# Kernel optimization log

Hardware: AMD Instinct MI355X
Metric: run time of the kernel (lower is better)

The kernel has to match this reference:

```python
import jax, jax.numpy as jnp
import numpy as np

B, S, D, H = 2, 2048, 1024, 16
HD = D // H  # head dim = 64


def setup_inputs() -> dict:
    key = jax.random.key(0)
    ks = jax.random.split(key, 11)
    s = 0.02
    return {
        "query": jax.random.normal(ks[0], (B, S, D), jnp.float32),
        "key": jax.random.normal(ks[1], (B, S, D), jnp.float32),
        "value": jax.random.normal(ks[2], (B, S, D), jnp.float32),
        "Wq": jax.random.normal(ks[3], (D, D), jnp.float32) * s,
        "bq": jnp.zeros((D,), jnp.float32),
        "Wk": jax.random.normal(ks[4], (D, D), jnp.float32) * s,
        "bk": jnp.zeros((D,), jnp.float32),
        "Wv": jax.random.normal(ks[5], (D, D), jnp.float32) * s,
        "bv": jnp.zeros((D,), jnp.float32),
        "Wo": jax.random.normal(ks[6], (D, D), jnp.float32) * s,
        "bo": jnp.zeros((D,), jnp.float32),
    }


def reference(query, key, value, Wq, bq, Wk, bk, Wv, bv, Wo, bo):
    # Linear projections (torch Linear: x @ W^T + b; here W stored as [in, out])
    q = query @ Wq + bq  # [B,S,D]
    k = key @ Wk + bk
    v = value @ Wv + bv
    # split heads -> [B,H,S,HD]
    q = q.reshape(B, S, H, HD).transpose(0, 2, 1, 3)
    k = k.reshape(B, S, H, HD).transpose(0, 2, 1, 3)
    v = v.reshape(B, S, H, HD).transpose(0, 2, 1, 3)
    scores = jnp.einsum("bhqd,bhkd->bhqk", q, k) / jnp.sqrt(jnp.float32(HD))
    probs = jax.nn.softmax(scores, axis=-1)
    # dropout is identity at inference
    ctx = jnp.einsum("bhqk,bhkd->bhqd", probs, v)
    ctx = ctx.transpose(0, 2, 1, 3).reshape(B, S, D)
    return ctx @ Wo + bo
```

## Files before the change

kernel.cpp:

```cpp
#include <hip/hip_runtime.h>
#include <hip/hip_bf16.h>

#define BB 2
#define SS 2048
#define DD 1024
#define HH 16
#define HD 64
#define MM (BB*SS)

typedef __attribute__((ext_vector_type(8))) short bf16x8;
typedef __attribute__((ext_vector_type(4))) float f32x4;

static __device__ inline unsigned short f2bf(float x) {
    unsigned int u = __float_as_uint(x);
    unsigned int r = (u + 0x7fffu + ((u >> 16) & 1u)) >> 16;
    return (unsigned short)r;
}

static __device__ inline unsigned pack2bf(float lo, float hi) {
    union { __hip_bfloat162 h; unsigned u; } c;
    c.h = __float22bfloat162_rn(make_float2(lo, hi));
    return c.u;
}

static __device__ inline f32x4 mfma16(bf16x8 a, bf16x8 b, f32x4 c) {
    return __builtin_amdgcn_mfma_f32_16x16x32_bf16(a, b, c, 0, 0, 0);
}

static __device__ inline float fast_exp2(float x) {
    return __builtin_amdgcn_exp2f(x);
}

typedef __attribute__((address_space(3))) unsigned int lds_u32;
typedef const __attribute__((address_space(1))) unsigned int glb_u32;
static __device__ inline void async_ld16(const void* g, void* l) {
    __builtin_amdgcn_global_load_lds((glb_u32*)g, (lds_u32*)l, 16, 0, 0);
}

struct PrepArgs {
    const float* csrc[3];
    unsigned short* cdst[3];
    const float* wsrc[4];
    unsigned short* wdst[4];
};
__global__ __launch_bounds__(256) void prep_inputs(PrepArgs args) {
    const int z = blockIdx.z;
    const int t = threadIdx.x;
    if (z < 3) {
        const float* in = args.csrc[z];
        unsigned short* out = args.cdst[z];
        int chunk = (blockIdx.y * 32 + blockIdx.x) * 4096;
#pragma unroll
        for (int r = 0; r < 4; r++) {
            int i = chunk + r * 1024 + t * 4;
            float4 v = *(const float4*)(in + i);
            uint2 o;
            o.x = pack2bf(v.x, v.y);
            o.y = pack2bf(v.z, v.w);
            *(uint2*)(out + i) = o;
        }
    } else {
        __shared__ float tile[32][33];
        const float* in = args.wsrc[z - 3];
        unsigned short* out = args.wdst[z - 3];
        int c0 = blockIdx.x * 32, r0 = blockIdx.y * 32;
        int x = t & 31, y0 = t >> 5;
        for (int yy = y0; yy < 32; yy += 8)
            tile[yy][x] = in[(size_t)(r0 + yy) * DD + c0 + x];
        __syncthreads();
        for (int yy = y0; yy < 32; yy += 8)
            out[(size_t)(c0 + yy) * DD + r0 + x] = f2bf(tile[x][yy]);
    }
}

struct QKVArgs {
    const unsigned short* A[3];
    const unsigned short* Bt[3];
    const float* bias[3];
    unsigned short* C[3];
};

#define QSCALE 0.1803368801111204f

#define NBUF 4
#define NT (DD / 32)

__global__ __launch_bounds__(512, 2) void gemm_qkv(QKVArgs args) {
    __shared__ alignas(16) unsigned short AS[NBUF][256 * 32];
    __shared__ alignas(16) unsigned short BS[NBUF][256 * 32];
    const int z = blockIdx.z;
    const float scale = (z == 0) ? QSCALE : 1.0f;
    const unsigned short* __restrict__ A = args.A[z];
    const unsigned short* __restrict__ Bt = args.Bt[z];
    const float* __restrict__ bias = args.bias[z];
    unsigned short* __restrict__ C = args.C[z];
    const int K = DD, N = DD;
    const int t = threadIdx.x;
    const int lane = t & 63, wave = t >> 6;
    const int quad = lane >> 4, l15 = lane & 15;
    const int wm = wave & 1, wn = wave >> 1;
    const int m0 = blockIdx.y * 256, n0 = blockIdx.x * 256;

    const int srow = wave * 16 + (lane >> 2);
    const int sslot = (lane & 3) ^ ((lane >> 3) & 3);
    const unsigned short* gA0 = A + (size_t)(m0 + srow) * K + sslot * 8;
    const unsigned short* gA1 = gA0 + (size_t)128 * K;
    const unsigned short* gB0 = Bt + (size_t)(n0 + srow) * K + sslot * 8;
    const unsigned short* gB1 = gB0 + (size_t)128 * K;
    const int rlo = wave * 512;
    const int rhi = wave * 512 + 4096;

    const int swzq = quad ^ ((l15 >> 1) & 3);

    auto stage = [&](int kt) {
        const int b = kt & (NBUF - 1);
        const size_t ko = (size_t)kt * 32;
        async_ld16(gA0 + ko, &AS[b][rlo]);
        async_ld16(gA1 + ko, &AS[b][rhi]);
        async_ld16(gB0 + ko, &BS[b][rlo]);
        async_ld16(gB1 + ko, &BS[b][rhi]);
    };

    stage(0); stage(1); stage(2);

    f32x4 acc[8][4];
#pragma unroll
    for (int i = 0; i < 8; i++)
#pragma unroll
        for (int j = 0; j < 4; j++) acc[i][j] = (f32x4){0.f, 0.f, 0.f, 0.f};

#pragma unroll 4
    for (int kt = 0; kt < NT; ++kt) {
        if (kt < NT - 2)       asm volatile("s_waitcnt vmcnt(8)" ::: "memory");
        else if (kt == NT - 2) asm volatile("s_waitcnt vmcnt(4)" ::: "memory");
        else                   asm volatile("s_waitcnt vmcnt(0)" ::: "memory");
        __builtin_amdgcn_s_barrier();
        if (kt + 3 < NT) stage(kt + 3);

        const unsigned short* Ab = AS[kt & (NBUF - 1)];
        const unsigned short* Bb = BS[kt & (NBUF - 1)];
        bf16x8 af[8], bfr[4];
#pragma unroll
        for (int i = 0; i < 8; i++)
            af[i] = *(const bf16x8*)&Ab[(wm * 128 + i * 16 + l15) * 32 + swzq * 8];
#pragma unroll
        for (int j = 0; j < 4; j++)
            bfr[j] = *(const bf16x8*)&Bb[(wn * 64 + j * 16 + l15) * 32 + swzq * 8];

        __builtin_amdgcn_s_setprio(1);
#pragma unroll
        for (int i = 0; i < 8; i++)
#pragma unroll
            for (int j = 0; j < 4; j++)
                acc[i][j] = mfma16(af[i], bfr[j], acc[i][j]);
        __builtin_amdgcn_s_setprio(0);
    }

    if (z == 2) {
#pragma unroll
        for (int j = 0; j < 4; j++) {
            int col = n0 + wn * 64 + j * 16 + l15;
            float bv = bias[col];
#pragma unroll
            for (int i = 0; i < 8; i++) {
                int rowb = m0 + wm * 128 + i * 16 + quad * 4;
                int b = rowb >> 11, s = rowb & (SS - 1);
                uint2 w;
                w.x = pack2bf(acc[i][j][0] + bv, acc[i][j][1] + bv);
                w.y = pack2bf(acc[i][j][2] + bv, acc[i][j][3] + bv);
                *(uint2*)(C + (size_t)b * DD * SS + (size_t)col * SS + s) = w;
            }
        }
    } else {
#pragma unroll
        for (int j = 0; j < 4; j++) {
            int col = n0 + wn * 64 + j * 16 + l15;
            float bv = bias[col];
#pragma unroll
            for (int i = 0; i < 8; i++) {
                int rowb = m0 + wm * 128 + i * 16 + quad * 4;
#pragma unroll
                for (int rr = 0; rr < 4; rr++) {
                    float v = (acc[i][j][rr] + bv) * scale;
                    C[(size_t)(rowb + rr) * N + col] = f2bf(v);
                }
            }
        }
    }
}

__global__ __launch_bounds__(256) void gemm_out(const unsigned short* __restrict__ A,
                                                const unsigned short* __restrict__ Bt,
                                                const float* __restrict__ bias,
                                                float* __restrict__ C) {
    __shared__ alignas(16) unsigned short As[128 * 32];
    __shared__ alignas(16) unsigned short Bs[64 * 32];
    const int t = threadIdx.x;
    const int lane = t & 63, wave = t >> 6;
    const int quad = lane >> 4, l15 = lane & 15;
    const int m0 = blockIdx.y * 128, n0 = blockIdx.x * 64;
    const int K = DD, N = DD;

    const unsigned short* gA = A + (size_t)(m0 + wave * 16 + (lane >> 2)) * K + (lane & 3) * 8;
    const unsigned short* gB = Bt + (size_t)(n0 + wave * 16 + (lane >> 2)) * K + (lane & 3) * 8;
    unsigned short* lA0 = &As[(wave * 16) * 32];
    unsigned short* lA1 = &As[(wave * 16 + 64) * 32];
    unsigned short* lB0 = &Bs[(wave * 16) * 32];

    f32x4 acc[2][4];
#pragma unroll
    for (int i = 0; i < 2; i++)
#pragma unroll
        for (int j = 0; j < 4; j++) acc[i][j] = (f32x4){0.f, 0.f, 0.f, 0.f};

    for (int k0 = 0; k0 < K; k0 += 32) {
        __syncthreads();
        async_ld16(gA + k0, lA0);
        async_ld16(gA + (size_t)64 * K + k0, lA1);
        async_ld16(gB + k0, lB0);
        __syncthreads();

        bf16x8 af[2], bfr[4];
#pragma unroll
        for (int i = 0; i < 2; i++)
            af[i] = *(const bf16x8*)&As[(wave * 32 + i * 16 + l15) * 32 + quad * 8];
#pragma unroll
        for (int j = 0; j < 4; j++)
            bfr[j] = *(const bf16x8*)&Bs[(j * 16 + l15) * 32 + quad * 8];
#pragma unroll
        for (int i = 0; i < 2; i++)
#pragma unroll
            for (int j = 0; j < 4; j++)
                acc[i][j] = mfma16(af[i], bfr[j], acc[i][j]);
    }

#pragma unroll
    for (int j = 0; j < 4; j++) {
        int col = n0 + j * 16 + l15;
        float bv = bias[col];
#pragma unroll
        for (int i = 0; i < 2; i++) {
            int rowb = m0 + wave * 32 + i * 16 + quad * 4;
#pragma unroll
            for (int rr = 0; rr < 4; rr++)
                C[(size_t)(rowb + rr) * N + col] = acc[i][j][rr] + bv;
        }
    }
}

#define TK 64
#define NTILE (SS / TK)
#define LDP 72

__global__ __launch_bounds__(256, 2) void flash_attn(const unsigned short* __restrict__ Q,
                                                     const unsigned short* __restrict__ Kg,
                                                     const unsigned short* __restrict__ Vt,
                                                     unsigned short* __restrict__ ctx) {
    __shared__ alignas(16) unsigned short Ks[2][TK * LDP];
    __shared__ alignas(16) unsigned short Vs[2][TK * LDP];
    const int t = threadIdx.x;
    const int lane = t & 63, wave = t >> 6;
    const int quad = lane >> 4, l15 = lane & 15;
    const int qg = blockIdx.x & 15;
    const int bh = blockIdx.x >> 4;
    const int h = bh & 15, b = bh >> 4;
    const int q0 = (qg * 4 + wave) * 32;

    const unsigned short* Qb = Q + (size_t)b * SS * DD + h * HD;
    const unsigned short* Kb = Kg + (size_t)b * SS * DD + h * HD;
    const unsigned short* Vb = Vt + ((size_t)b * DD + h * HD) * SS;

    const int r0 = t >> 3, cs = t & 7;
    const unsigned short* gK = Kb + (size_t)r0 * DD + cs * 8;
    const unsigned short* gV = Vb + (size_t)r0 * SS + cs * 8;
    const int ldsoff0 = r0 * LDP + cs * 8;
    const int ldsoff1 = (r0 + 32) * LDP + cs * 8;

    bf16x8 qa[2][2];
#pragma unroll
    for (int qt = 0; qt < 2; qt++) {
        qa[qt][0] = *(const bf16x8*)(Qb + (size_t)(q0 + qt * 16 + l15) * DD + quad * 8);
        qa[qt][1] = *(const bf16x8*)(Qb + (size_t)(q0 + qt * 16 + l15) * DD + 32 + quad * 8);
    }

    float lrow[2] = {0.f, 0.f};
    f32x4 o[2][4];
#pragma unroll
    for (int qt = 0; qt < 2; qt++)
#pragma unroll
        for (int j = 0; j < 4; j++) o[qt][j] = (f32x4){0.f, 0.f, 0.f, 0.f};

    {
        uint4 kr0 = *(const uint4*)(gK);
        uint4 kr1 = *(const uint4*)(gK + (size_t)32 * DD);
        uint4 vr0 = *(const uint4*)(gV);
        uint4 vr1 = *(const uint4*)(gV + (size_t)32 * SS);
        *(uint4*)&Ks[0][ldsoff0] = kr0;
        *(uint4*)&Ks[0][ldsoff1] = kr1;
        *(uint4*)&Vs[0][ldsoff0] = vr0;
        *(uint4*)&Vs[0][ldsoff1] = vr1;
    }
    __syncthreads();

    for (int tile = 0; tile < NTILE; ++tile) {
        const int buf = tile & 1;
        uint4 kr0, kr1, vr0, vr1;
        if (tile + 1 < NTILE) {
            const unsigned short* gKn = gK + (size_t)(tile + 1) * TK * DD;
            const unsigned short* gVn = gV + (tile + 1) * TK;
            kr0 = *(const uint4*)(gKn);
            kr1 = *(const uint4*)(gKn + (size_t)32 * DD);
            vr0 = *(const uint4*)(gVn);
            vr1 = *(const uint4*)(gVn + (size_t)32 * SS);
        }
        const unsigned short* Ksb = Ks[buf];
        const unsigned short* Vsb = Vs[buf];
#pragma unroll
        for (int half = 0; half < 2; half++) {
            const int kb0 = half * 32;
            bf16x8 k0 = *(const bf16x8*)&Ksb[(kb0 + l15) * LDP + quad * 8];
            bf16x8 k1 = *(const bf16x8*)&Ksb[(kb0 + l15) * LDP + 32 + quad * 8];
            bf16x8 k2 = *(const bf16x8*)&Ksb[(kb0 + 16 + l15) * LDP + quad * 8];
            bf16x8 k3 = *(const bf16x8*)&Ksb[(kb0 + 16 + l15) * LDP + 32 + quad * 8];
            union { ushort4 s[2]; bf16x8 v; } af[4];
#pragma unroll
            for (int j = 0; j < 4; j++) {
                af[j].s[0] = *(const ushort4*)&Vsb[(j * 16 + l15) * LDP + kb0 + quad * 4];
                af[j].s[1] = *(const ushort4*)&Vsb[(j * 16 + l15) * LDP + kb0 + 16 + quad * 4];
            }
#pragma unroll
            for (int qt = 0; qt < 2; qt++) {
                f32x4 sc0 = (f32x4){0.f, 0.f, 0.f, 0.f};
                f32x4 sc1 = (f32x4){0.f, 0.f, 0.f, 0.f};
                sc0 = mfma16(k0, qa[qt][0], sc0);
                sc0 = mfma16(k1, qa[qt][1], sc0);
                sc1 = mfma16(k2, qa[qt][0], sc1);
                sc1 = mfma16(k3, qa[qt][1], sc1);

                float p[8];
#pragma unroll
                for (int rr = 0; rr < 4; rr++) {
                    p[rr]     = fast_exp2(sc0[rr]);
                    p[rr + 4] = fast_exp2(sc1[rr]);
                }
                lrow[qt] += (p[0] + p[1]) + (p[2] + p[3]) + (p[4] + p[5]) + (p[6] + p[7]);

                union { unsigned u[4]; bf16x8 v; } pf;
                pf.u[0] = pack2bf(p[0], p[1]);
                pf.u[1] = pack2bf(p[2], p[3]);
                pf.u[2] = pack2bf(p[4], p[5]);
                pf.u[3] = pack2bf(p[6], p[7]);

#pragma unroll
                for (int j = 0; j < 4; j++)
                    o[qt][j] = mfma16(af[j].v, pf.v, o[qt][j]);
            }
        }
        if (tile + 1 < NTILE) {
            __syncthreads();
            *(uint4*)&Ks[buf ^ 1][ldsoff0] = kr0;
            *(uint4*)&Ks[buf ^ 1][ldsoff1] = kr1;
            *(uint4*)&Vs[buf ^ 1][ldsoff0] = vr0;
            *(uint4*)&Vs[buf ^ 1][ldsoff1] = vr1;
            __syncthreads();
        }
    }

#pragma unroll
    for (int qt = 0; qt < 2; qt++) {
        float l = lrow[qt];
        l += __shfl_xor(l, 16, 64);
        l += __shfl_xor(l, 32, 64);
        float linv = 1.0f / l;
        unsigned short* crow = ctx + ((size_t)b * SS + q0 + qt * 16 + l15) * DD + h * HD;
#pragma unroll
        for (int j = 0; j < 4; j++) {
            uint2 w;
            w.x = pack2bf(o[qt][j][0] * linv, o[qt][j][1] * linv);
            w.y = pack2bf(o[qt][j][2] * linv, o[qt][j][3] * linv);
            *(uint2*)(crow + j * 16 + quad * 4) = w;
        }
    }
}

extern "C" void kernel_launch(void* const* d_in, const int* in_sizes, int n_in,
                              void* d_out, int out_size, void* d_ws, size_t ws_size,
                              hipStream_t stream) {
    const float* query = (const float*)d_in[0];
    const float* key   = (const float*)d_in[1];
    const float* value = (const float*)d_in[2];
    const float* Wq = (const float*)d_in[3];
    const float* bq = (const float*)d_in[4];
    const float* Wk = (const float*)d_in[5];
    const float* bk = (const float*)d_in[6];
    const float* Wv = (const float*)d_in[7];
    const float* bv = (const float*)d_in[8];
    const float* Wo = (const float*)d_in[9];
    const float* bo = (const float*)d_in[10];
    float* out = (float*)d_out;

    char* ws = (char*)d_ws;
    const size_t WSZ = (size_t)DD * DD * 2;
    const size_t XSZ = (size_t)MM * DD * 2;
    unsigned short* Wqt = (unsigned short*)(ws + 0 * WSZ);
    unsigned short* Wkt = (unsigned short*)(ws + 1 * WSZ);
    unsigned short* Wvt = (unsigned short*)(ws + 2 * WSZ);
    unsigned short* Wot = (unsigned short*)(ws + 3 * WSZ);
    unsigned short* Xq  = (unsigned short*)(ws + 4 * WSZ);
    unsigned short* Xk  = (unsigned short*)(ws + 4 * WSZ + 1 * XSZ);
    unsigned short* Xv  = (unsigned short*)(ws + 4 * WSZ + 2 * XSZ);
    unsigned short* Qp  = (unsigned short*)(ws + 4 * WSZ + 3 * XSZ);
    unsigned short* Kp  = (unsigned short*)(ws + 4 * WSZ + 4 * XSZ);
    unsigned short* Vtp = (unsigned short*)(ws + 4 * WSZ + 5 * XSZ);
    unsigned short* ctx = Xk;

    PrepArgs pargs;
    pargs.csrc[0] = query; pargs.csrc[1] = key; pargs.csrc[2] = value;
    pargs.cdst[0] = Xq; pargs.cdst[1] = Xk; pargs.cdst[2] = Xv;
    pargs.wsrc[0] = Wq; pargs.wsrc[1] = Wk; pargs.wsrc[2] = Wv; pargs.wsrc[3] = Wo;
    pargs.wdst[0] = Wqt; pargs.wdst[1] = Wkt; pargs.wdst[2] = Wvt; pargs.wdst[3] = Wot;
    prep_inputs<<<dim3(32, 32, 7), 256, 0, stream>>>(pargs);

    QKVArgs args;
    args.A[0] = Xq; args.A[1] = Xk; args.A[2] = Xv;
    args.Bt[0] = Wqt; args.Bt[1] = Wkt; args.Bt[2] = Wvt;
    args.bias[0] = bq; args.bias[1] = bk; args.bias[2] = bv;
    args.C[0] = Qp; args.C[1] = Kp; args.C[2] = Vtp;
    gemm_qkv<<<dim3(DD / 256, MM / 256, 3), 512, 0, stream>>>(args);

    flash_attn<<<BB * HH * 16, 256, 0, stream>>>(Qp, Kp, Vtp, ctx);

    gemm_out<<<dim3(DD / 64, MM / 128), 256, 0, stream>>>(ctx, Wot, bo, out);
}
```

Before: 230.8 us.

## Halve per-wave query rows in flash attention, doubling grid and occupancy

Each wave now handles 16 query rows instead of 32, so the attention grid doubles to 1024 blocks and launch bounds rise to 4 blocks per CU. This is meant to improve latency hiding and fill the GPU better. The cost is that every K/V tile loaded into LDS is reused by half as many query rows, doubling global and LDS traffic per unit of work. The MFMA sections are also wrapped in s_setprio to raise wave priority during matrix math.

```diff
diff --git a/kernel.cpp b/kernel.cpp
--- a/kernel.cpp
+++ b/kernel.cpp
@@ -252,7 +252,7 @@
 #define NTILE (SS / TK)
 #define LDP 72
 
-__global__ __launch_bounds__(256, 2) void flash_attn(const unsigned short* __restrict__ Q,
+__global__ __launch_bounds__(256, 4) void flash_attn(const unsigned short* __restrict__ Q,
                                                      const unsigned short* __restrict__ Kg,
                                                      const unsigned short* __restrict__ Vt,
                                                      unsigned short* __restrict__ ctx) {
@@ -261,10 +261,10 @@
     const int t = threadIdx.x;
     const int lane = t & 63, wave = t >> 6;
     const int quad = lane >> 4, l15 = lane & 15;
-    const int qg = blockIdx.x & 15;
-    const int bh = blockIdx.x >> 4;
+    const int qg = blockIdx.x & 31;
+    const int bh = blockIdx.x >> 5;
     const int h = bh & 15, b = bh >> 4;
-    const int q0 = (qg * 4 + wave) * 32;
+    const int q0 = (qg * 4 + wave) * 16;
 
     const unsigned short* Qb = Q + (size_t)b * SS * DD + h * HD;
     const unsigned short* Kb = Kg + (size_t)b * SS * DD + h * HD;
@@ -276,19 +276,13 @@
     const int ldsoff0 = r0 * LDP + cs * 8;
     const int ldsoff1 = (r0 + 32) * LDP + cs * 8;
 
-    bf16x8 qa[2][2];
-#pragma unroll
-    for (int qt = 0; qt < 2; qt++) {
-        qa[qt][0] = *(const bf16x8*)(Qb + (size_t)(q0 + qt * 16 + l15) * DD + quad * 8);
-        qa[qt][1] = *(const bf16x8*)(Qb + (size_t)(q0 + qt * 16 + l15) * DD + 32 + quad * 8);
-    }
-
-    float lrow[2] = {0.f, 0.f};
-    f32x4 o[2][4];
-#pragma unroll
-    for (int qt = 0; qt < 2; qt++)
-#pragma unroll
-        for (int j = 0; j < 4; j++) o[qt][j] = (f32x4){0.f, 0.f, 0.f, 0.f};
+    bf16x8 qa0 = *(const bf16x8*)(Qb + (size_t)(q0 + l15) * DD + quad * 8);
+    bf16x8 qa1 = *(const bf16x8*)(Qb + (size_t)(q0 + l15) * DD + 32 + quad * 8);
+
+    float lrow = 0.f;
+    f32x4 o[4];
+#pragma unroll
+    for (int j = 0; j < 4; j++) o[j] = (f32x4){0.f, 0.f, 0.f, 0.f};
 
     {
         uint4 kr0 = *(const uint4*)(gK);
@@ -328,33 +322,34 @@
                 af[j].s[0] = *(const ushort4*)&Vsb[(j * 16 + l15) * LDP + kb0 + quad * 4];
                 af[j].s[1] = *(const ushort4*)&Vsb[(j * 16 + l15) * LDP + kb0 + 16 + quad * 4];
             }
-#pragma unroll
-            for (int qt = 0; qt < 2; qt++) {
-                f32x4 sc0 = (f32x4){0.f, 0.f, 0.f, 0.f};
-                f32x4 sc1 = (f32x4){0.f, 0.f, 0.f, 0.f};
-                sc0 = mfma16(k0, qa[qt][0], sc0);
-                sc0 = mfma16(k1, qa[qt][1], sc0);
-                sc1 = mfma16(k2, qa[qt][0], sc1);
-                sc1 = mfma16(k3, qa[qt][1], sc1);
-
-                float p[8];
-#pragma unroll
-                for (int rr = 0; rr < 4; rr++) {
-                    p[rr]     = fast_exp2(sc0[rr]);
-                    p[rr + 4] = fast_exp2(sc1[rr]);
-                }
-                lrow[qt] += (p[0] + p[1]) + (p[2] + p[3]) + (p[4] + p[5]) + (p[6] + p[7]);
-
-                union { unsigned u[4]; bf16x8 v; } pf;
-                pf.u[0] = pack2bf(p[0], p[1]);
-                pf.u[1] = pack2bf(p[2], p[3]);
-                pf.u[2] = pack2bf(p[4], p[5]);
-                pf.u[3] = pack2bf(p[6], p[7]);
-
-#pragma unroll
-                for (int j = 0; j < 4; j++)
-                    o[qt][j] = mfma16(af[j].v, pf.v, o[qt][j]);
+            f32x4 sc0 = (f32x4){0.f, 0.f, 0.f, 0.f};
+            f32x4 sc1 = (f32x4){0.f, 0.f, 0.f, 0.f};
+            __builtin_amdgcn_s_setprio(1);
+            sc0 = mfma16(k0, qa0, sc0);
+            sc0 = mfma16(k1, qa1, sc0);
+            sc1 = mfma16(k2, qa0, sc1);
+            sc1 = mfma16(k3, qa1, sc1);
+            __builtin_amdgcn_s_setprio(0);
+
+            float p[8];
+#pragma unroll
+            for (int rr = 0; rr < 4; rr++) {
+                p[rr]     = fast_exp2(sc0[rr]);
+                p[rr + 4] = fast_exp2(sc1[rr]);
             }
+            lrow += (p[0] + p[1]) + (p[2] + p[3]) + (p[4] + p[5]) + (p[6] + p[7]);
+
+            union { unsigned u[4]; bf16x8 v; } pf;
+            pf.u[0] = pack2bf(p[0], p[1]);
+            pf.u[1] = pack2bf(p[2], p[3]);
+            pf.u[2] = pack2bf(p[4], p[5]);
+            pf.u[3] = pack2bf(p[6], p[7]);
+
+            __builtin_amdgcn_s_setprio(1);
+#pragma unroll
+            for (int j = 0; j < 4; j++)
+                o[j] = mfma16(af[j].v, pf.v, o[j]);
+            __builtin_amdgcn_s_setprio(0);
         }
         if (tile + 1 < NTILE) {
             __syncthreads();
@@ -366,18 +361,17 @@
         }
     }
 
-#pragma unroll
-    for (int qt = 0; qt < 2; qt++) {
-        float l = lrow[qt];
+    {
+        float l = lrow;
         l += __shfl_xor(l, 16, 64);
         l += __shfl_xor(l, 32, 64);
         float linv = 1.0f / l;
-        unsigned short* crow = ctx + ((size_t)b * SS + q0 + qt * 16 + l15) * DD + h * HD;
+        unsigned short* crow = ctx + ((size_t)b * SS + q0 + l15) * DD + h * HD;
 #pragma unroll
         for (int j = 0; j < 4; j++) {
             uint2 w;
-            w.x = pack2bf(o[qt][j][0] * linv, o[qt][j][1] * linv);
-            w.y = pack2bf(o[qt][j][2] * linv, o[qt][j][3] * linv);
+            w.x = pack2bf(o[j][0] * linv, o[j][1] * linv);
+            w.y = pack2bf(o[j][2] * linv, o[j][3] * linv);
             *(uint2*)(crow + j * 16 + quad * 4) = w;
         }
     }
@@ -428,7 +422,7 @@
     args.C[0] = Qp; args.C[1] = Kp; args.C[2] = Vtp;
     gemm_qkv<<<dim3(DD / 256, MM / 256, 3), 512, 0, stream>>>(args);
 
-    flash_attn<<<BB * HH * 16, 256, 0, stream>>>(Qp, Kp, Vtp, ctx);
+    flash_attn<<<BB * HH * 32, 256, 0, stream>>>(Qp, Kp, Vtp, ctx);
 
     gemm_out<<<dim3(DD / 64, MM / 128), 256, 0, stream>>>(ctx, Wot, bo, out);
 }
```

Measured after the change: 233.8 us. Within noise of the previous version (+1.3%).

## Load V fragments directly from global memory, remap blocks, add MFMA priority

Applied to the files above, without the earlier changes.

The V tile no longer goes through LDS. Each lane now reads its MFMA A-fragment for V straight from global memory (the transposed Vt, 8-byte loads) inside the compute loop. This halves shared memory use and the LDS store traffic, at the cost of uncoalesced, latency-exposed global loads that depend on L2/cache hits. The block index is also remapped so consecutive blocks spread across (b,h) groups, likely to improve XCD/L2 locality. s_setprio is raised around the MFMA sections to favour matrix issue.

```diff
diff --git a/kernel.cpp b/kernel.cpp
--- a/kernel.cpp
+++ b/kernel.cpp
@@ -257,12 +257,12 @@
                                                      const unsigned short* __restrict__ Vt,
                                                      unsigned short* __restrict__ ctx) {
     __shared__ alignas(16) unsigned short Ks[2][TK * LDP];
-    __shared__ alignas(16) unsigned short Vs[2][TK * LDP];
     const int t = threadIdx.x;
     const int lane = t & 63, wave = t >> 6;
     const int quad = lane >> 4, l15 = lane & 15;
-    const int qg = blockIdx.x & 15;
-    const int bh = blockIdx.x >> 4;
+    const int wg = (blockIdx.x & 7) * 64 + (blockIdx.x >> 3);
+    const int qg = wg & 15;
+    const int bh = wg >> 4;
     const int h = bh & 15, b = bh >> 4;
     const int q0 = (qg * 4 + wave) * 32;
 
@@ -272,9 +272,13 @@
 
     const int r0 = t >> 3, cs = t & 7;
     const unsigned short* gK = Kb + (size_t)r0 * DD + cs * 8;
-    const unsigned short* gV = Vb + (size_t)r0 * SS + cs * 8;
     const int ldsoff0 = r0 * LDP + cs * 8;
     const int ldsoff1 = (r0 + 32) * LDP + cs * 8;
+
+    const unsigned short* gV0 = Vb + (size_t)(0 * 16 + l15) * SS + quad * 4;
+    const unsigned short* gV1 = Vb + (size_t)(1 * 16 + l15) * SS + quad * 4;
+    const unsigned short* gV2 = Vb + (size_t)(2 * 16 + l15) * SS + quad * 4;
+    const unsigned short* gV3 = Vb + (size_t)(3 * 16 + l15) * SS + quad * 4;
 
     bf16x8 qa[2][2];
 #pragma unroll
@@ -293,28 +297,21 @@
     {
         uint4 kr0 = *(const uint4*)(gK);
         uint4 kr1 = *(const uint4*)(gK + (size_t)32 * DD);
-        uint4 vr0 = *(const uint4*)(gV);
-        uint4 vr1 = *(const uint4*)(gV + (size_t)32 * SS);
         *(uint4*)&Ks[0][ldsoff0] = kr0;
         *(uint4*)&Ks[0][ldsoff1] = kr1;
-        *(uint4*)&Vs[0][ldsoff0] = vr0;
-        *(uint4*)&Vs[0][ldsoff1] = vr1;
     }
     __syncthreads();
 
     for (int tile = 0; tile < NTILE; ++tile) {
         const int buf = tile & 1;
-        uint4 kr0, kr1, vr0, vr1;
+        uint4 kr0, kr1;
         if (tile + 1 < NTILE) {
             const unsigned short* gKn = gK + (size_t)(tile + 1) * TK * DD;
-            const unsigned short* gVn = gV + (tile + 1) * TK;
             kr0 = *(const uint4*)(gKn);
             kr1 = *(const uint4*)(gKn + (size_t)32 * DD);
-            vr0 = *(const uint4*)(gVn);
-            vr1 = *(const uint4*)(gVn + (size_t)32 * SS);
         }
         const unsigned short* Ksb = Ks[buf];
-        const unsigned short* Vsb = Vs[buf];
+        const int vcol = tile * TK;
 #pragma unroll
         for (int half = 0; half < 2; half++) {
             const int kb0 = half * 32;
@@ -323,19 +320,24 @@
             bf16x8 k2 = *(const bf16x8*)&Ksb[(kb0 + 16 + l15) * LDP + quad * 8];
             bf16x8 k3 = *(const bf16x8*)&Ksb[(kb0 + 16 + l15) * LDP + 32 + quad * 8];
             union { ushort4 s[2]; bf16x8 v; } af[4];
-#pragma unroll
-            for (int j = 0; j < 4; j++) {
-                af[j].s[0] = *(const ushort4*)&Vsb[(j * 16 + l15) * LDP + kb0 + quad * 4];
-                af[j].s[1] = *(const ushort4*)&Vsb[(j * 16 + l15) * LDP + kb0 + 16 + quad * 4];
-            }
+            af[0].s[0] = *(const ushort4*)(gV0 + vcol + kb0);
+            af[0].s[1] = *(const ushort4*)(gV0 + vcol + kb0 + 16);
+            af[1].s[0] = *(const ushort4*)(gV1 + vcol + kb0);
+            af[1].s[1] = *(const ushort4*)(gV1 + vcol + kb0 + 16);
+            af[2].s[0] = *(const ushort4*)(gV2 + vcol + kb0);
+            af[2].s[1] = *(const ushort4*)(gV2 + vcol + kb0 + 16);
+            af[3].s[0] = *(const ushort4*)(gV3 + vcol + kb0);
+            af[3].s[1] = *(const ushort4*)(gV3 + vcol + kb0 + 16);
 #pragma unroll
             for (int qt = 0; qt < 2; qt++) {
                 f32x4 sc0 = (f32x4){0.f, 0.f, 0.f, 0.f};
                 f32x4 sc1 = (f32x4){0.f, 0.f, 0.f, 0.f};
+                __builtin_amdgcn_s_setprio(1);
                 sc0 = mfma16(k0, qa[qt][0], sc0);
                 sc0 = mfma16(k1, qa[qt][1], sc0);
                 sc1 = mfma16(k2, qa[qt][0], sc1);
                 sc1 = mfma16(k3, qa[qt][1], sc1);
+                __builtin_amdgcn_s_setprio(0);
 
                 float p[8];
 #pragma unroll
@@ -351,17 +353,17 @@
                 pf.u[2] = pack2bf(p[4], p[5]);
                 pf.u[3] = pack2bf(p[6], p[7]);
 
+                __builtin_amdgcn_s_setprio(1);
 #pragma unroll
                 for (int j = 0; j < 4; j++)
                     o[qt][j] = mfma16(af[j].v, pf.v, o[qt][j]);
+                __builtin_amdgcn_s_setprio(0);
             }
         }
         if (tile + 1 < NTILE) {
             __syncthreads();
             *(uint4*)&Ks[buf ^ 1][ldsoff0] = kr0;
             *(uint4*)&Ks[buf ^ 1][ldsoff1] = kr1;
-            *(uint4*)&Vs[buf ^ 1][ldsoff0] = vr0;
-            *(uint4*)&Vs[buf ^ 1][ldsoff1] = vr1;
             __syncthreads();
         }
     }
```

New measurement: 300.1 us. +30.0%, slower.

## Interleave LDS fragment loads and async global prefetch with MFMA sub-blocks in GEMM loop

Applied to the files above, without the earlier changes.

The GEMM main loop is split into four MFMA phases, each preceded by a partial LDS fragment load and one of the four async global-to-LDS prefetches, with a workgroup barrier between phases. The goal is to overlap LDS reads and global loads with matrix-core work and to cut the live fragment registers (af drops from 8 to 4). The cost is extra barriers per iteration, which can stall waves, and a less flexible instruction schedule for the compiler.

```diff
diff --git a/kernel.cpp b/kernel.cpp
--- a/kernel.cpp
+++ b/kernel.cpp
@@ -112,7 +112,7 @@
 
     const int swzq = quad ^ ((l15 >> 1) & 3);
 
-    auto stage = [&](int kt) {
+    auto stage_all = [&](int kt) {
         const int b = kt & (NBUF - 1);
         const size_t ko = (size_t)kt * 32;
         async_ld16(gA0 + ko, &AS[b][rlo]);
@@ -121,7 +121,7 @@
         async_ld16(gB1 + ko, &BS[b][rhi]);
     };
 
-    stage(0); stage(1); stage(2);
+    stage_all(0); stage_all(1); stage_all(2);
 
     f32x4 acc[8][4];
 #pragma unroll
@@ -134,25 +134,65 @@
         if (kt < NT - 2)       asm volatile("s_waitcnt vmcnt(8)" ::: "memory");
         else if (kt == NT - 2) asm volatile("s_waitcnt vmcnt(4)" ::: "memory");
         else                   asm volatile("s_waitcnt vmcnt(0)" ::: "memory");
-        __builtin_amdgcn_s_barrier();
-        if (kt + 3 < NT) stage(kt + 3);
-
+        asm volatile("s_barrier" ::: "memory");
+
+        const bool pf = (kt + 3 < NT);
+        const int bb = (kt + 3) & (NBUF - 1);
+        const size_t ko = (size_t)(kt + 3) * 32;
         const unsigned short* Ab = AS[kt & (NBUF - 1)];
         const unsigned short* Bb = BS[kt & (NBUF - 1)];
-        bf16x8 af[8], bfr[4];
-#pragma unroll
-        for (int i = 0; i < 8; i++)
+        bf16x8 af[4], bfr[4];
+
+#pragma unroll
+        for (int j = 0; j < 2; j++)
+            bfr[j] = *(const bf16x8*)&Bb[(wn * 64 + j * 16 + l15) * 32 + swzq * 8];
+#pragma unroll
+        for (int i = 0; i < 4; i++)
             af[i] = *(const bf16x8*)&Ab[(wm * 128 + i * 16 + l15) * 32 + swzq * 8];
-#pragma unroll
-        for (int j = 0; j < 4; j++)
+        if (pf) async_ld16(gA0 + ko, &AS[bb][rlo]);
+        asm volatile("s_barrier" ::: "memory");
+        __builtin_amdgcn_s_setprio(1);
+#pragma unroll
+        for (int i = 0; i < 4; i++) {
+            acc[i][0] = mfma16(af[i], bfr[0], acc[i][0]);
+            acc[i][1] = mfma16(af[i], bfr[1], acc[i][1]);
+        }
+        __builtin_amdgcn_s_setprio(0);
+
+#pragma unroll
+        for (int j = 2; j < 4; j++)
             bfr[j] = *(const bf16x8*)&Bb[(wn * 64 + j * 16 + l15) * 32 + swzq * 8];
-
+        if (pf) async_ld16(gA1 + ko, &AS[bb][rhi]);
+        asm volatile("s_barrier" ::: "memory");
         __builtin_amdgcn_s_setprio(1);
 #pragma unroll
-        for (int i = 0; i < 8; i++)
-#pragma unroll
-            for (int j = 0; j < 4; j++)
-                acc[i][j] = mfma16(af[i], bfr[j], acc[i][j]);
+        for (int i = 0; i < 4; i++) {
+            acc[i][2] = mfma16(af[i], bfr[2], acc[i][2]);
+            acc[i][3] = mfma16(af[i], bfr[3], acc[i][3]);
+        }
+        __builtin_amdgcn_s_setprio(0);
+
+#pragma unroll
+        for (int i = 0; i < 4; i++)
+            af[i] = *(const bf16x8*)&Ab[(wm * 128 + 64 + i * 16 + l15) * 32 + swzq * 8];
+        if (pf) async_ld16(gB0 + ko, &BS[bb][rlo]);
+        asm volatile("s_barrier" ::: "memory");
+        __builtin_amdgcn_s_setprio(1);
+#pragma unroll
+        for (int i = 0; i < 4; i++) {
+            acc[4 + i][0] = mfma16(af[i], bfr[0], acc[4 + i][0]);
+            acc[4 + i][1] = mfma16(af[i], bfr[1], acc[4 + i][1]);
+        }
+        __builtin_amdgcn_s_setprio(0);
+
+        if (pf) async_ld16(gB1 + ko, &BS[bb][rhi]);
+        asm volatile("s_barrier" ::: "memory");
+        __builtin_amdgcn_s_setprio(1);
+#pragma unroll
+        for (int i = 0; i < 4; i++) {
+            acc[4 + i][2] = mfma16(af[i], bfr[2], acc[4 + i][2]);
+            acc[4 + i][3] = mfma16(af[i], bfr[3], acc[4 + i][3]);
+        }
         __builtin_amdgcn_s_setprio(0);
     }
 
```

Result: no change. 232.8 us (+0.9%).
